# Performance work log

Measured on AMD Instinct MI355X. Metric: run time of the kernel, lower is better.

Reference implementation:

```python
import jax, jax.numpy as jnp
import numpy as np

E = 8        # n_experts
TOP_K = 2    # top_k_experts


def setup_inputs() -> dict:
    key = jax.random.key(0)
    ks = jax.random.split(key, 4)
    B, N, D, H = 4, 2048, 1024, 1024
    s_d = 1.0 / np.sqrt(D)
    s_h = 1.0 / np.sqrt(H)
    return {
        "x": jax.random.normal(ks[0], (B, N, D), dtype=jnp.float32),
        "router_w": jax.random.normal(ks[1], (E, D), dtype=jnp.float32) * s_d,
        "router_b": jnp.zeros((E,), dtype=jnp.float32),
        "W_up": jax.random.normal(ks[2], (E, D, H), dtype=jnp.float32) * s_d,
        "b_up": jnp.zeros((E, H), dtype=jnp.float32),
        "W_down": jax.random.normal(ks[3], (E, H, D), dtype=jnp.float32) * s_h,
        "b_down": jnp.zeros((E, D), dtype=jnp.float32),
    }


def reference(x, router_w, router_b, W_up, b_up, W_down, b_down):
    # Router logits: (B, N, E)
    logits = jnp.einsum("bnd,ed->bne", x, router_w) + router_b
    _, topk_idx = jax.lax.top_k(logits, TOP_K)          # (B, N, K)
    # Boolean mask of selected experts: (B, N, E)
    mask = jax.nn.one_hot(topk_idx, E, dtype=jnp.bool_).any(axis=-2)
    masked_logits = jnp.where(mask, logits, -jnp.inf)
    router_weights = jax.nn.softmax(masked_logits, axis=-1)  # zeros off top-k
    # Dense all-experts FFN: (B, N, E, H) intermediate
    h = jnp.einsum("bnd,edh->bneh", x, W_up) + b_up
    h = jax.nn.gelu(h, approximate=False)  # torch F.gelu default = exact erf
    h = jnp.einsum("bneh,ehd->bned", h, W_down) + b_down
    output = jnp.einsum("bne,bned->bnd", router_weights, h)
    # Switch load-balancing aux loss (dropout is identity in eval)
    f_i = mask.astype(x.dtype).mean(axis=(0, 1))
    P_i = router_weights.mean(axis=(0, 1))
    aux_loss = E * jnp.sum(f_i * P_i)
    return output, aux_loss
```

## Files before the change

kernel.cpp:

```cpp
#include <hip/hip_runtime.h>
#include <hip/hip_bf16.h>

typedef __attribute__((ext_vector_type(8))) short bf16x8_t;
typedef __attribute__((ext_vector_type(4))) float f32x4_t;

__device__ __forceinline__ void gld16(void* lds, const void* g) {
    __builtin_amdgcn_global_load_lds(
        (const __attribute__((address_space(1))) void*)g,
        (__attribute__((address_space(3))) void*)lds, 16, 0, 0);
}

__device__ inline unsigned short f2bf(float f) {
    __hip_bfloat16 h = __float2bfloat16(f);
    return *reinterpret_cast<unsigned short*>(&h);
}

#define VM_WAIT4() asm volatile("s_waitcnt vmcnt(4)" ::: "memory")
#define VM_WAIT0() asm volatile("s_waitcnt vmcnt(0)" ::: "memory")
#define SCHED_FENCE() __builtin_amdgcn_sched_barrier(0)

__global__ __launch_bounds__(256) void transpose_kernel(
    const float* __restrict__ Wup, const float* __restrict__ Wdn,
    ushort* __restrict__ WtUp, ushort* __restrict__ WtDn)
{
    int z = blockIdx.z;
    const float* src = (z < 8) ? (Wup + ((size_t)z << 20)) : (Wdn + ((size_t)(z - 8) << 20));
    ushort* dst      = (z < 8) ? (WtUp + ((size_t)z << 20)) : (WtDn + ((size_t)(z - 8) << 20));
    __shared__ float tile[64][65];
    int x0 = blockIdx.x * 64, y0 = blockIdx.y * 64;
    int row = threadIdx.x >> 4, colq = threadIdx.x & 15;
#pragma unroll
    for (int it = 0; it < 4; it++) {
        int r = row + it * 16;
        float4 v = *(const float4*)(src + (size_t)(y0 + r) * 1024 + x0 + colq * 4);
        tile[r][colq * 4 + 0] = v.x; tile[r][colq * 4 + 1] = v.y;
        tile[r][colq * 4 + 2] = v.z; tile[r][colq * 4 + 3] = v.w;
    }
    __syncthreads();
#pragma unroll
    for (int it = 0; it < 4; it++) {
        int r = row + it * 16;
        ushort4 o;
        o.x = f2bf(tile[colq * 4 + 0][r]); o.y = f2bf(tile[colq * 4 + 1][r]);
        o.z = f2bf(tile[colq * 4 + 2][r]); o.w = f2bf(tile[colq * 4 + 3][r]);
        *(ushort4*)(dst + (size_t)(x0 + r) * 1024 + y0 + colq * 4) = o;
    }
}

__global__ __launch_bounds__(256) void router_kernel(
    const float* __restrict__ x, const float* __restrict__ rw,
    const float* __restrict__ rb, ushort* __restrict__ xb,
    int2* __restrict__ tok_e, float2* __restrict__ tok_w)
{
    int wave = threadIdx.x >> 6, lane = threadIdx.x & 63;
    int t = blockIdx.x * 4 + wave;
    float4 xv[4];
#pragma unroll
    for (int i = 0; i < 4; i++)
        xv[i] = *(const float4*)(x + (size_t)t * 1024 + i * 256 + lane * 4);
#pragma unroll
    for (int i = 0; i < 4; i++) {
        ushort4 o;
        o.x = f2bf(xv[i].x); o.y = f2bf(xv[i].y); o.z = f2bf(xv[i].z); o.w = f2bf(xv[i].w);
        *(ushort4*)(xb + (size_t)t * 1024 + i * 256 + lane * 4) = o;
    }
    float logit[8];
#pragma unroll
    for (int e = 0; e < 8; e++) {
        float s = 0.f;
#pragma unroll
        for (int i = 0; i < 4; i++) {
            float4 wv = *(const float4*)(rw + e * 1024 + i * 256 + lane * 4);
            s += xv[i].x * wv.x + xv[i].y * wv.y + xv[i].z * wv.z + xv[i].w * wv.w;
        }
#pragma unroll
        for (int m = 32; m >= 1; m >>= 1) s += __shfl_xor(s, m, 64);
        logit[e] = s + rb[e];
    }
    int i0 = 0;
#pragma unroll
    for (int e = 1; e < 8; e++) if (logit[e] > logit[i0]) i0 = e;
    int i1 = -1;
#pragma unroll
    for (int e = 0; e < 8; e++) if (e != i0 && (i1 < 0 || logit[e] > logit[i1])) i1 = e;
    float ev = expf(logit[i1] - logit[i0]);
    float s = 1.f + ev;
    if (lane == 0) {
        tok_e[t] = make_int2(i0, i1);
        tok_w[t] = make_float2(1.f / s, ev / s);
    }
}

__global__ __launch_bounds__(256) void count_kernel(
    const int2* __restrict__ tok_e, const float2* __restrict__ tok_w,
    int* __restrict__ blockCnt, float* __restrict__ blockSum)
{
    __shared__ int lcnt[8];
    __shared__ float lsum[8];
    int tid = threadIdx.x;
    if (tid < 8) { lcnt[tid] = 0; lsum[tid] = 0.f; }
    __syncthreads();
    int t = blockIdx.x * 256 + tid;
    int2 e = tok_e[t]; float2 w = tok_w[t];
    atomicAdd(&lcnt[e.x], 1); atomicAdd(&lsum[e.x], w.x);
    atomicAdd(&lcnt[e.y], 1); atomicAdd(&lsum[e.y], w.y);
    __syncthreads();
    if (tid < 8) {
        blockCnt[blockIdx.x * 8 + tid] = lcnt[tid];
        blockSum[blockIdx.x * 8 + tid] = lsum[tid];
    }
}

__global__ void scan_kernel(const int* __restrict__ blockCnt,
                            const float* __restrict__ blockSum,
                            int* __restrict__ cnt, int* __restrict__ off,
                            int* __restrict__ base, int* __restrict__ tileE,
                            int* __restrict__ tileRow, int* __restrict__ nTiles,
                            float* aux_out)
{
    if (threadIdx.x == 0) {
        int tot[8]; float sw[8];
        for (int e = 0; e < 8; e++) { tot[e] = 0; sw[e] = 0.f; }
        for (int b = 0; b < 32; b++)
            for (int e = 0; e < 8; e++) { tot[e] += blockCnt[b * 8 + e]; sw[e] += blockSum[b * 8 + e]; }
        int o = 0; float aux = 0.f; int nT = 0;
        for (int e = 0; e < 8; e++) {
            cnt[e] = tot[e]; off[e] = o;
            aux += (float)tot[e] * sw[e];
            int run = o;
            for (int b = 0; b < 32; b++) { base[b * 8 + e] = run; run += blockCnt[b * 8 + e]; }
            for (int tt = 0; tt * 128 < tot[e]; tt++) { tileE[nT] = e; tileRow[nT] = o + tt * 128; nT++; }
            o += tot[e];
        }
        *nTiles = nT;
        aux *= 8.0f / (8192.0f * 8192.0f);
        *aux_out = aux;
    }
}

__global__ __launch_bounds__(256) void assign_kernel(
    const int2* __restrict__ tok_e, const float2* __restrict__ tok_w,
    const int* __restrict__ base, int* __restrict__ pair_token,
    float* __restrict__ pair_w, int2* __restrict__ tokSlot)
{
    __shared__ int lcnt[8];
    int tid = threadIdx.x;
    if (tid < 8) lcnt[tid] = 0;
    __syncthreads();
    int t = blockIdx.x * 256 + tid;
    int2 e = tok_e[t]; float2 w = tok_w[t];
    int r0 = atomicAdd(&lcnt[e.x], 1);
    int r1 = atomicAdd(&lcnt[e.y], 1);
    int s0 = base[blockIdx.x * 8 + e.x] + r0;
    int s1 = base[blockIdx.x * 8 + e.y] + r1;
    pair_token[s0] = t; pair_w[s0] = w.x;
    pair_token[s1] = t; pair_w[s1] = w.y;
    tokSlot[t] = make_int2(s0, s1);
}

#define STAGE(buf, kk_) do {                               \
    gld16(&As[buf][(w * 16) * 32],        aP0 + (kk_));    \
    gld16(&As[buf][(64 + w * 16) * 32],   aP1 + (kk_));    \
    gld16(&Bs[buf][(w * 16) * 32],        bP0 + (kk_));    \
    gld16(&Bs[buf][(64 + w * 16) * 32],   bP1 + (kk_));    \
} while (0)

#define COMPUTE_STEP(cur_) do {                                                              \
    bf16x8_t a[4], b[4];                                                                     \
    _Pragma("unroll")                                                                        \
    for (int i = 0; i < 4; i++) a[i] = *(const bf16x8_t*)&As[cur_][(wm * 64 + i * 16 + r) * 32 + q * 8]; \
    _Pragma("unroll")                                                                        \
    for (int j = 0; j < 4; j++) b[j] = *(const bf16x8_t*)&Bs[cur_][(wn * 64 + j * 16 + r) * 32 + q * 8]; \
    _Pragma("unroll")                                                                        \
    for (int i = 0; i < 4; i++)                                                              \
        _Pragma("unroll")                                                                    \
        for (int j = 0; j < 4; j++)                                                          \
            acc[i][j] = __builtin_amdgcn_mfma_f32_16x16x32_bf16(a[i], b[j], acc[i][j], 0, 0, 0); \
} while (0)

__global__ __launch_bounds__(256) void up_gemm(
    const ushort* __restrict__ xb, const ushort* __restrict__ WtUp,
    const float* __restrict__ bup,
    const int* __restrict__ cnt, const int* __restrict__ off,
    const int* __restrict__ nTiles, const int* __restrict__ tileE,
    const int* __restrict__ tileRow,
    const int* __restrict__ pair_token, const float* __restrict__ pair_w,
    const ushort* __restrict__ zeroPage, ushort* __restrict__ Hbuf)
{
    if ((int)blockIdx.y >= *nTiles) return;
    int e = tileE[blockIdx.y];
    int rowBase = tileRow[blockIdx.y];
    int expertEnd = off[e] + cnt[e];
    int colBase = blockIdx.x * 128;
    const ushort* Bsrc = WtUp + ((size_t)e << 20);

    __shared__ __align__(16) ushort smem[16384];
    ushort (*As)[4096] = (ushort (*)[4096])smem;
    ushort (*Bs)[4096] = (ushort (*)[4096])(smem + 8192);

    int tid = threadIdx.x, w = tid >> 6, lane = tid & 63;
    int q = lane >> 4, r = lane & 15;
    int wm = w & 1, wn = w >> 1;

    int sr = lane >> 2;
    int cOff = (lane & 3) * 8;
    int rA0 = w * 16 + sr, rA1 = 64 + w * 16 + sr;
    int gA0 = rowBase + rA0, gA1 = rowBase + rA1;

    const ushort* aP0 = (gA0 < expertEnd) ? xb + (size_t)pair_token[gA0] * 1024 + cOff : zeroPage + cOff;
    const ushort* aP1 = (gA1 < expertEnd) ? xb + (size_t)pair_token[gA1] * 1024 + cOff : zeroPage + cOff;
    const ushort* bP0 = Bsrc + (size_t)(colBase + rA0) * 1024 + cOff;
    const ushort* bP1 = Bsrc + (size_t)(colBase + rA1) * 1024 + cOff;

    f32x4_t acc[4][4];
#pragma unroll
    for (int i = 0; i < 4; i++)
#pragma unroll
        for (int j = 0; j < 4; j++) { acc[i][j][0] = 0.f; acc[i][j][1] = 0.f; acc[i][j][2] = 0.f; acc[i][j][3] = 0.f; }

    STAGE(0, 0);
    int cur = 0;
#pragma unroll 2
    for (int kk = 0; kk < 992; kk += 32) {
        STAGE(cur ^ 1, kk + 32);
        VM_WAIT4();
        __builtin_amdgcn_s_barrier();
        SCHED_FENCE();
        COMPUTE_STEP(cur);
        SCHED_FENCE();
        __builtin_amdgcn_s_barrier();
        cur ^= 1;
    }
    VM_WAIT0();
    __builtin_amdgcn_s_barrier();
    SCHED_FENCE();
    COMPUTE_STEP(cur);

    float biasv[4];
#pragma unroll
    for (int j = 0; j < 4; j++) biasv[j] = bup[e * 1024 + colBase + wn * 64 + j * 16 + r];
#pragma unroll
    for (int half = 0; half < 2; half++) {
        __syncthreads();
        if (wm == half) {
#pragma unroll
            for (int i = 0; i < 4; i++) {
#pragma unroll
                for (int reg = 0; reg < 4; reg++) {
                    int lr = i * 16 + q * 4 + reg;
                    int gRow = rowBase + half * 64 + lr;
                    float pw = (gRow < expertEnd) ? pair_w[gRow] : 0.f;
#pragma unroll
                    for (int j = 0; j < 4; j++) {
                        float h = acc[i][j][reg] + biasv[j];
                        float g = 0.5f * h * (1.0f + erff(h * 0.70710678118654752f));
                        smem[lr * 136 + wn * 64 + j * 16 + r] = f2bf(g * pw);
                    }
                }
            }
        }
        __syncthreads();
#pragma unroll
        for (int n = 0; n < 4; n++) {
            int lr = n * 16 + (tid >> 4);
            int gRow = rowBase + half * 64 + lr;
            if (gRow < expertEnd) {
                bf16x8_t v = *(const bf16x8_t*)&smem[lr * 136 + (tid & 15) * 8];
                *(bf16x8_t*)(Hbuf + (size_t)gRow * 1024 + colBase + (tid & 15) * 8) = v;
            }
        }
    }
}

__global__ __launch_bounds__(256) void down_gemm(
    const ushort* __restrict__ Hbuf, const ushort* __restrict__ WtDn,
    const int* __restrict__ cnt, const int* __restrict__ off,
    const int* __restrict__ nTiles, const int* __restrict__ tileE,
    const int* __restrict__ tileRow,
    const ushort* __restrict__ zeroPage, ushort* __restrict__ pairOut)
{
    if ((int)blockIdx.y >= *nTiles) return;
    int e = tileE[blockIdx.y];
    int rowBase = tileRow[blockIdx.y];
    int expertEnd = off[e] + cnt[e];
    int colBase = blockIdx.x * 128;
    const ushort* Bsrc = WtDn + ((size_t)e << 20);

    __shared__ __align__(16) ushort smem[16384];
    ushort (*As)[4096] = (ushort (*)[4096])smem;
    ushort (*Bs)[4096] = (ushort (*)[4096])(smem + 8192);

    int tid = threadIdx.x, w = tid >> 6, lane = tid & 63;
    int q = lane >> 4, r = lane & 15;
    int wm = w & 1, wn = w >> 1;

    int sr = lane >> 2;
    int cOff = (lane & 3) * 8;
    int rA0 = w * 16 + sr, rA1 = 64 + w * 16 + sr;
    int gA0 = rowBase + rA0, gA1 = rowBase + rA1;

    const ushort* aP0 = (gA0 < expertEnd) ? Hbuf + (size_t)gA0 * 1024 + cOff : zeroPage + cOff;
    const ushort* aP1 = (gA1 < expertEnd) ? Hbuf + (size_t)gA1 * 1024 + cOff : zeroPage + cOff;
    const ushort* bP0 = Bsrc + (size_t)(colBase + rA0) * 1024 + cOff;
    const ushort* bP1 = Bsrc + (size_t)(colBase + rA1) * 1024 + cOff;

    f32x4_t acc[4][4];
#pragma unroll
    for (int i = 0; i < 4; i++)
#pragma unroll
        for (int j = 0; j < 4; j++) { acc[i][j][0] = 0.f; acc[i][j][1] = 0.f; acc[i][j][2] = 0.f; acc[i][j][3] = 0.f; }

    STAGE(0, 0);
    int cur = 0;
#pragma unroll 2
    for (int kk = 0; kk < 992; kk += 32) {
        STAGE(cur ^ 1, kk + 32);
        VM_WAIT4();
        __builtin_amdgcn_s_barrier();
        SCHED_FENCE();
        COMPUTE_STEP(cur);
        SCHED_FENCE();
        __builtin_amdgcn_s_barrier();
        cur ^= 1;
    }
    VM_WAIT0();
    __builtin_amdgcn_s_barrier();
    SCHED_FENCE();
    COMPUTE_STEP(cur);

#pragma unroll
    for (int half = 0; half < 2; half++) {
        __syncthreads();
        if (wm == half) {
#pragma unroll
            for (int i = 0; i < 4; i++) {
#pragma unroll
                for (int reg = 0; reg < 4; reg++) {
                    int lr = i * 16 + q * 4 + reg;
#pragma unroll
                    for (int j = 0; j < 4; j++)
                        smem[lr * 136 + wn * 64 + j * 16 + r] = f2bf(acc[i][j][reg]);
                }
            }
        }
        __syncthreads();
#pragma unroll
        for (int n = 0; n < 4; n++) {
            int lr = n * 16 + (tid >> 4);
            int gRow = rowBase + half * 64 + lr;
            if (gRow < expertEnd) {
                bf16x8_t v = *(const bf16x8_t*)&smem[lr * 136 + (tid & 15) * 8];
                *(bf16x8_t*)(pairOut + (size_t)gRow * 1024 + colBase + (tid & 15) * 8) = v;
            }
        }
    }
}

__global__ __launch_bounds__(256) void finalize_kernel(
    const ushort* __restrict__ pairOut, const int2* __restrict__ tokSlot,
    const int2* __restrict__ tok_e, const float2* __restrict__ tok_w,
    const float* __restrict__ bdn, float* __restrict__ out)
{
    int t = blockIdx.x;
    int2 s = tokSlot[t]; int2 e = tok_e[t]; float2 w = tok_w[t];
    int c = threadIdx.x * 4;
    ushort4 p0 = *(const ushort4*)(pairOut + (size_t)s.x * 1024 + c);
    ushort4 p1 = *(const ushort4*)(pairOut + (size_t)s.y * 1024 + c);
    float4 b0 = *(const float4*)(bdn + (size_t)e.x * 1024 + c);
    float4 b1 = *(const float4*)(bdn + (size_t)e.y * 1024 + c);
    __hip_bfloat16* h0 = (__hip_bfloat16*)&p0;
    __hip_bfloat16* h1 = (__hip_bfloat16*)&p1;
    float4 o;
    o.x = __bfloat162float(h0[0]) + __bfloat162float(h1[0]) + w.x * b0.x + w.y * b1.x;
    o.y = __bfloat162float(h0[1]) + __bfloat162float(h1[1]) + w.x * b0.y + w.y * b1.y;
    o.z = __bfloat162float(h0[2]) + __bfloat162float(h1[2]) + w.x * b0.z + w.y * b1.z;
    o.w = __bfloat162float(h0[3]) + __bfloat162float(h1[3]) + w.x * b0.w + w.y * b1.w;
    *(float4*)(out + (size_t)t * 1024 + c) = o;
}

extern "C" void kernel_launch(void* const* d_in, const int* in_sizes, int n_in,
                              void* d_out, int out_size, void* d_ws, size_t ws_size,
                              hipStream_t stream) {
    const float* x   = (const float*)d_in[0];
    const float* rw  = (const float*)d_in[1];
    const float* rb  = (const float*)d_in[2];
    const float* Wup = (const float*)d_in[3];
    const float* bup = (const float*)d_in[4];
    const float* Wdn = (const float*)d_in[5];
    const float* bdn = (const float*)d_in[6];
    float* out = (float*)d_out;

    char* ws = (char*)d_ws;
    int*    cnt      = (int*)(ws + 0);
    int*    off      = (int*)(ws + 64);
    int*    nTiles   = (int*)(ws + 128);
    int*    blockCnt = (int*)(ws + 256);
    float*  blockSum = (float*)(ws + 1536);
    int*    base     = (int*)(ws + 2816);
    int*    tileE    = (int*)(ws + 4096);
    int*    tileRow  = (int*)(ws + 4736);
    ushort* zeroPage = (ushort*)(ws + 8192);
    int2*   tok_e    = (int2*)(ws + 12288);
    float2* tok_w    = (float2*)(ws + 77824);
    int2*   tokSlot  = (int2*)(ws + 143360);
    int*    pair_token = (int*)(ws + 208896);
    float*  pair_w     = (float*)(ws + 274432);
    char* big = ws + 1048576;
    ushort* Hbuf    = (ushort*)big;
    ushort* pairOut = (ushort*)(big + 33554432);
    ushort* WtUp    = (ushort*)(big + 67108864);
    ushort* WtDn    = (ushort*)(big + 83886080);
    ushort* xb      = (ushort*)(big + 100663296);

    hipMemsetAsync(zeroPage, 0, 4096, stream);

    transpose_kernel<<<dim3(16, 16, 16), 256, 0, stream>>>(Wup, Wdn, WtUp, WtDn);
    router_kernel<<<2048, 256, 0, stream>>>(x, rw, rb, xb, tok_e, tok_w);
    count_kernel<<<32, 256, 0, stream>>>(tok_e, tok_w, blockCnt, blockSum);
    scan_kernel<<<1, 64, 0, stream>>>(blockCnt, blockSum, cnt, off, base,
                                      tileE, tileRow, nTiles, out + 8388608);
    assign_kernel<<<32, 256, 0, stream>>>(tok_e, tok_w, base, pair_token, pair_w, tokSlot);
    up_gemm<<<dim3(8, 136), 256, 0, stream>>>(
        xb, WtUp, bup, cnt, off, nTiles, tileE, tileRow, pair_token, pair_w, zeroPage, Hbuf);
    down_gemm<<<dim3(8, 136), 256, 0, stream>>>(
        Hbuf, WtDn, cnt, off, nTiles, tileE, tileRow, zeroPage, pairOut);
    finalize_kernel<<<8192, 256, 0, stream>>>(pairOut, tokSlot, tok_e, tok_w, bdn, out);
}
```

Measured before the change: 338.9 us.

## Swizzle tile-column block mapping and restructure double-buffered K loop with syncthreads

```diff
diff --git a/kernel.cpp b/kernel.cpp
--- a/kernel.cpp
+++ b/kernel.cpp
@@ -14,10 +14,6 @@
     __hip_bfloat16 h = __float2bfloat16(f);
     return *reinterpret_cast<unsigned short*>(&h);
 }
-
-#define VM_WAIT4() asm volatile("s_waitcnt vmcnt(4)" ::: "memory")
-#define VM_WAIT0() asm volatile("s_waitcnt vmcnt(0)" ::: "memory")
-#define SCHED_FENCE() __builtin_amdgcn_sched_barrier(0)
 
 __global__ __launch_bounds__(256) void transpose_kernel(
     const float* __restrict__ Wup, const float* __restrict__ Wdn,
@@ -165,18 +161,25 @@
     gld16(&Bs[buf][(64 + w * 16) * 32],   bP1 + (kk_));    \
 } while (0)
 
-#define COMPUTE_STEP(cur_) do {                                                              \
+#define COMPUTE_STEP(buf_) do {                                                              \
     bf16x8_t a[4], b[4];                                                                     \
     _Pragma("unroll")                                                                        \
-    for (int i = 0; i < 4; i++) a[i] = *(const bf16x8_t*)&As[cur_][(wm * 64 + i * 16 + r) * 32 + q * 8]; \
+    for (int i = 0; i < 4; i++) a[i] = *(const bf16x8_t*)&As[buf_][(wm * 64 + i * 16 + r) * 32 + q * 8]; \
     _Pragma("unroll")                                                                        \
-    for (int j = 0; j < 4; j++) b[j] = *(const bf16x8_t*)&Bs[cur_][(wn * 64 + j * 16 + r) * 32 + q * 8]; \
+    for (int j = 0; j < 4; j++) b[j] = *(const bf16x8_t*)&Bs[buf_][(wn * 64 + j * 16 + r) * 32 + q * 8]; \
     _Pragma("unroll")                                                                        \
     for (int i = 0; i < 4; i++)                                                              \
         _Pragma("unroll")                                                                    \
         for (int j = 0; j < 4; j++)                                                          \
             acc[i][j] = __builtin_amdgcn_mfma_f32_16x16x32_bf16(a[i], b[j], acc[i][j], 0, 0, 0); \
 } while (0)
+
+__device__ __forceinline__ void swz_tile_col(int& tileId, int& colBlk) {
+    int lin = blockIdx.y * 8 + blockIdx.x;
+    int swz = (lin & 7) * 136 + (lin >> 3);
+    tileId = swz >> 3;
+    colBlk = swz & 7;
+}
 
 __global__ __launch_bounds__(256) void up_gemm(
     const ushort* __restrict__ xb, const ushort* __restrict__ WtUp,
@@ -187,11 +190,13 @@
     const int* __restrict__ pair_token, const float* __restrict__ pair_w,
     const ushort* __restrict__ zeroPage, ushort* __restrict__ Hbuf)
 {
-    if ((int)blockIdx.y >= *nTiles) return;
-    int e = tileE[blockIdx.y];
-    int rowBase = tileRow[blockIdx.y];
+    int tileId, colBlk;
+    swz_tile_col(tileId, colBlk);
+    if (tileId >= *nTiles) return;
+    int e = tileE[tileId];
+    int rowBase = tileRow[tileId];
     int expertEnd = off[e] + cnt[e];
-    int colBase = blockIdx.x * 128;
+    int colBase = colBlk * 128;
     const ushort* Bsrc = WtUp + ((size_t)e << 20);
 
     __shared__ __align__(16) ushort smem[16384];
@@ -219,22 +224,16 @@
         for (int j = 0; j < 4; j++) { acc[i][j][0] = 0.f; acc[i][j][1] = 0.f; acc[i][j][2] = 0.f; acc[i][j][3] = 0.f; }
 
     STAGE(0, 0);
-    int cur = 0;
-#pragma unroll 2
-    for (int kk = 0; kk < 992; kk += 32) {
-        STAGE(cur ^ 1, kk + 32);
-        VM_WAIT4();
-        __builtin_amdgcn_s_barrier();
-        SCHED_FENCE();
-        COMPUTE_STEP(cur);
-        SCHED_FENCE();
-        __builtin_amdgcn_s_barrier();
-        cur ^= 1;
-    }
-    VM_WAIT0();
-    __builtin_amdgcn_s_barrier();
-    SCHED_FENCE();
-    COMPUTE_STEP(cur);
+    __syncthreads();
+#pragma unroll 1
+    for (int kk = 0; kk < 1024; kk += 64) {
+        STAGE(1, kk + 32);
+        COMPUTE_STEP(0);
+        __syncthreads();
+        if (kk + 64 < 1024) STAGE(0, kk + 64);
+        COMPUTE_STEP(1);
+        __syncthreads();
+    }
 
     float biasv[4];
 #pragma unroll
@@ -279,11 +278,13 @@
     const int* __restrict__ tileRow,
     const ushort* __restrict__ zeroPage, ushort* __restrict__ pairOut)
 {
-    if ((int)blockIdx.y >= *nTiles) return;
-    int e = tileE[blockIdx.y];
-    int rowBase = tileRow[blockIdx.y];
+    int tileId, colBlk;
+    swz_tile_col(tileId, colBlk);
+    if (tileId >= *nTiles) return;
+    int e = tileE[tileId];
+    int rowBase = tileRow[tileId];
     int expertEnd = off[e] + cnt[e];
-    int colBase = blockIdx.x * 128;
+    int colBase = colBlk * 128;
     const ushort* Bsrc = WtDn + ((size_t)e << 20);
 
     __shared__ __align__(16) ushort smem[16384];
@@ -311,22 +312,16 @@
         for (int j = 0; j < 4; j++) { acc[i][j][0] = 0.f; acc[i][j][1] = 0.f; acc[i][j][2] = 0.f; acc[i][j][3] = 0.f; }
 
     STAGE(0, 0);
-    int cur = 0;
-#pragma unroll 2
-    for (int kk = 0; kk < 992; kk += 32) {
-        STAGE(cur ^ 1, kk + 32);
-        VM_WAIT4();
-        __builtin_amdgcn_s_barrier();
-        SCHED_FENCE();
-        COMPUTE_STEP(cur);
-        SCHED_FENCE();
-        __builtin_amdgcn_s_barrier();
-        cur ^= 1;
-    }
-    VM_WAIT0();
-    __builtin_amdgcn_s_barrier();
-    SCHED_FENCE();
-    COMPUTE_STEP(cur);
+    __syncthreads();
+#pragma unroll 1
+    for (int kk = 0; kk < 1024; kk += 64) {
+        STAGE(1, kk + 32);
+        COMPUTE_STEP(0);
+        __syncthreads();
+        if (kk + 64 < 1024) STAGE(0, kk + 64);
+        COMPUTE_STEP(1);
+        __syncthreads();
+    }
 
 #pragma unroll
     for (int half = 0; half < 2; half++) {
```

New measurement: 332.0 us. -2.0%, faster.
